# Optimization experiments

Measured on AMD Instinct MI355X. Metric: run time of the kernel, lower is better.

Reference implementation:

```python
import jax, jax.numpy as jnp
import numpy as np

BITS = 4
MAXQ = 15            # 2**BITS - 1
PACK = 32 // BITS    # 8 int4 values per int32
GROUPSIZE = 128
M, K, N = 2048, 4096, 4096
G = K // GROUPSIZE


def setup_inputs() -> dict:
    key = jax.random.key(0)
    k1, k2, k3, k4, k5 = jax.random.split(key, 5)
    x = jax.random.normal(k1, (M, K), dtype=jnp.float32)
    qweight = jax.random.randint(k2, (K // PACK, N), 0, 2147483647, dtype=jnp.int32)
    qzeros = jax.random.randint(k3, (G, N // PACK), 0, 2147483647, dtype=jnp.int32)
    scales = jax.random.uniform(k4, (G, N), dtype=jnp.float32) * 0.01
    g_idx = (jnp.arange(K, dtype=jnp.int32) // GROUPSIZE).astype(jnp.int32)
    bias = jax.random.normal(k5, (N,), dtype=jnp.float32)
    return {"x": x, "qweight": qweight, "qzeros": qzeros,
            "scales": scales, "g_idx": g_idx, "bias": bias}


def _dequantize(qweight, qzeros, scales, g_idx):
    shifts = (jnp.arange(PACK, dtype=jnp.int32) * BITS)
    # unpack weights along K: [K//8, N] -> [K//8, 8, N] -> [K, N]
    w_int = ((qweight[:, None, :] >> shifts[None, :, None]) & MAXQ)
    w_int = w_int.reshape(K, N)
    # unpack zeros along N: [G, N//8] -> [G, N//8, 8] -> [G, N]; kernel adds 1
    z_int = ((qzeros[:, :, None] >> shifts[None, None, :]) & MAXQ) + 1
    z_int = z_int.reshape(G, N)
    # group-wise dequant: W[k, n] = (w - zeros[g_idx[k]]) * scales[g_idx[k]]
    W = (w_int - z_int[g_idx]).astype(jnp.float32) * scales[g_idx]
    return W  # [K, N]


def reference(x, qweight, qzeros, scales, g_idx, bias):
    W = _dequantize(qweight, qzeros, scales, g_idx)
    return x @ W + bias  # [M, N]
```

## Files before the change

### kernel.cpp

```cpp
#include <hip/hip_runtime.h>
#include <hip/hip_bf16.h>
#include <stdint.h>

#define M_DIM 2048
#define K_DIM 4096
#define N_DIM 4096

typedef __attribute__((ext_vector_type(8))) short short8;
typedef __attribute__((ext_vector_type(4))) float f32x4;

#define MFMA __builtin_amdgcn_mfma_f32_16x16x32_bf16

__device__ __forceinline__ uint32_t bf16pk(float a, float b) {
  uint32_t ua = __float_as_uint(a);
  ua = (ua + 0x7FFFu + ((ua >> 16) & 1u)) >> 16;
  uint32_t ub = __float_as_uint(b);
  ub = (ub + 0x7FFFu + ((ub >> 16) & 1u)) >> 16;
  return ua | (ub << 16);
}

__device__ __forceinline__ void glds16(const char* g, char* l) {
  __builtin_amdgcn_global_load_lds((__attribute__((address_space(1))) void*)g,
                                   (__attribute__((address_space(3))) void*)l, 16, 0, 0);
}


__global__ void __launch_bounds__(256) cvt_x_kernel(const float* __restrict__ x,
                                                    char* __restrict__ xImg) {
  const int mt = blockIdx.x >> 6, kt = blockIdx.x & 63;
  const int tid = threadIdx.x;
  const int k8 = tid & 7, rbase = tid >> 3;
  const float* xb = x + (size_t)mt * 256 * K_DIM + kt * 64 + k8 * 8;
  char* ob = xImg + (size_t)(mt * 64 + kt) * 32768 + k8 * 4096;
#pragma unroll
  for (int j = 0; j < 8; ++j) {
    int row = j * 32 + rbase;
    const float* src = xb + (size_t)row * K_DIM;
    float4 f0 = *(const float4*)src;
    float4 f1 = *(const float4*)(src + 4);
    uint4 pk;
    pk.x = bf16pk(f0.x, f0.y);
    pk.y = bf16pk(f0.z, f0.w);
    pk.z = bf16pk(f1.x, f1.y);
    pk.w = bf16pk(f1.z, f1.w);
    *(uint4*)(ob + row * 16) = pk;
  }
}

__global__ void __launch_bounds__(256) deq_w_kernel(const uint32_t* __restrict__ qweight,
                                                    const uint32_t* __restrict__ qzeros,
                                                    const float* __restrict__ scales,
                                                    char* __restrict__ wImg) {
  const int nt = blockIdx.x >> 6, kt = blockIdx.x & 63;
  const int t = threadIdx.x;
  const int n = nt * 256 + t;
  const int g = kt >> 1;
  uint32_t zq = qzeros[g * (N_DIM / 8) + (n >> 3)];
  const int z = (int)((zq >> ((n & 7) * 4)) & 15u) + 1;
  const float s = scales[g * N_DIM + n];
  char* ob = wImg + (size_t)(nt * 64 + kt) * 32768;
#pragma unroll
  for (int slot = 0; slot < 8; ++slot) {
    uint32_t q = qweight[(size_t)(kt * 8 + slot) * N_DIM + n];
    float f[8];
#pragma unroll
    for (int v = 0; v < 8; ++v) {
      int w = (int)((q >> (4 * v)) & 15u);
      f[v] = (float)(w - z) * s;
    }
    uint4 pk;
    pk.x = bf16pk(f[0], f[1]);
    pk.y = bf16pk(f[2], f[3]);
    pk.z = bf16pk(f[4], f[5]);
    pk.w = bf16pk(f[6], f[7]);
    *(uint4*)(ob + slot * 4096 + t * 16) = pk;
  }
}

__global__ void __launch_bounds__(512, 2) gemm_kernel(const char* __restrict__ xImg,
                                                      const char* __restrict__ wImg,
                                                      const float* __restrict__ bias,
                                                      float* __restrict__ out,
                                                      float* __restrict__ part1) {
  __shared__ uint4 ldsv[8192];
  char* lds = (char*)ldsv;
  const int tid = threadIdx.x;
  const int lane = tid & 63, wid = tid >> 6;
  const int wr = wid >> 2, wc = wid & 3;
  const int lr = lane & 15, lk = lane >> 4;

  const int bid = blockIdx.x;
  const int i5 = bid >> 3;
  const int nb = (bid & 7) * 2 + (i5 & 1);
  const int mb = (i5 >> 1) & 7;
  const int ks = i5 >> 4;

  f32x4 acc[8][4];
#pragma unroll
  for (int i = 0; i < 8; ++i)
#pragma unroll
    for (int j = 0; j < 4; ++j) acc[i][j] = f32x4{0.f, 0.f, 0.f, 0.f};

  const char* aT = xImg + (size_t)(mb * 128 + ks * 64) * 16384;
  const char* bT = wImg + (size_t)(nb * 128 + ks * 64) * 16384;

  int aoff[8], boff[4];
#pragma unroll
  for (int i = 0; i < 8; ++i) aoff[i] = lk * 4096 + (wr * 128 + i * 16 + lr) * 16;
#pragma unroll
  for (int j = 0; j < 4; ++j) boff[j] = 16384 + lk * 4096 + (wc * 64 + j * 16 + lr) * 16;

#define STG(src, dstoff)                                                 \
  do {                                                                   \
    glds16((src) + tid * 16, lds + (dstoff) + tid * 16);                 \
    glds16((src) + 8192 + tid * 16, lds + (dstoff) + 8192 + tid * 16);   \
  } while (0)

  STG(aT, 0);                STG(bT, 16384);
  STG(aT + 16384, 32768);    STG(bT + 16384, 32768 + 16384);
  STG(aT + 32768, 65536);    STG(bT + 32768, 65536 + 16384);
  asm volatile("s_waitcnt vmcnt(8)" ::: "memory");
  __builtin_amdgcn_sched_barrier(0);
  __builtin_amdgcn_s_barrier();

  short8 a0 = *(const short8*)(lds + aoff[0]);
  short8 a1 = *(const short8*)(lds + aoff[1]);
  short8 a2 = *(const short8*)(lds + aoff[2]);
  short8 a3 = *(const short8*)(lds + aoff[3]);
  short8 b0 = *(const short8*)(lds + boff[0]);
  short8 b1 = *(const short8*)(lds + boff[1]);

#pragma unroll 4
  for (int t = 0; t < 64; ++t) {
    const char* buf  = lds + (t & 3) * 32768;
    const char* bufn = lds + ((t + 1) & 3) * 32768;
    const int nso = ((t + 3) & 3) * 32768;
    const char* aN = aT + (size_t)(t + 3) * 16384;
    const char* bN = bT + (size_t)(t + 3) * 16384;

    short8 b2 = *(const short8*)(buf + boff[2]);
    short8 b3 = *(const short8*)(buf + boff[3]);
    short8 a4 = *(const short8*)(buf + aoff[4]);
    short8 a5 = *(const short8*)(buf + aoff[5]);
    short8 a6 = *(const short8*)(buf + aoff[6]);
    short8 a7 = *(const short8*)(buf + aoff[7]);
    if (t <= 60) STG(aN, nso);
    __builtin_amdgcn_sched_barrier(0);
    __builtin_amdgcn_s_barrier();
    asm volatile("s_waitcnt lgkmcnt(6)" ::: "memory");
    __builtin_amdgcn_sched_barrier(0);
    __builtin_amdgcn_s_setprio(1);
    acc[0][0] = MFMA(a0, b0, acc[0][0], 0, 0, 0);
    acc[1][0] = MFMA(a1, b0, acc[1][0], 0, 0, 0);
    acc[2][0] = MFMA(a2, b0, acc[2][0], 0, 0, 0);
    acc[3][0] = MFMA(a3, b0, acc[3][0], 0, 0, 0);
    acc[0][1] = MFMA(a0, b1, acc[0][1], 0, 0, 0);
    acc[1][1] = MFMA(a1, b1, acc[1][1], 0, 0, 0);
    acc[2][1] = MFMA(a2, b1, acc[2][1], 0, 0, 0);
    acc[3][1] = MFMA(a3, b1, acc[3][1], 0, 0, 0);
    asm volatile("s_waitcnt lgkmcnt(4)" ::: "memory");
    __builtin_amdgcn_sched_barrier(0);
    acc[0][2] = MFMA(a0, b2, acc[0][2], 0, 0, 0);
    acc[1][2] = MFMA(a1, b2, acc[1][2], 0, 0, 0);
    acc[2][2] = MFMA(a2, b2, acc[2][2], 0, 0, 0);
    acc[3][2] = MFMA(a3, b2, acc[3][2], 0, 0, 0);
    acc[0][3] = MFMA(a0, b3, acc[0][3], 0, 0, 0);
    acc[1][3] = MFMA(a1, b3, acc[1][3], 0, 0, 0);
    acc[2][3] = MFMA(a2, b3, acc[2][3], 0, 0, 0);
    acc[3][3] = MFMA(a3, b3, acc[3][3], 0, 0, 0);
    __builtin_amdgcn_s_setprio(0);
    if (t <= 60)      asm volatile("s_waitcnt vmcnt(6)" ::: "memory");
    else if (t == 61) asm volatile("s_waitcnt vmcnt(4)" ::: "memory");
    else if (t == 62) asm volatile("s_waitcnt vmcnt(0)" ::: "memory");
    __builtin_amdgcn_sched_barrier(0);
    __builtin_amdgcn_s_barrier();
    __builtin_amdgcn_sched_barrier(0);

    short8 na0 = *(const short8*)(bufn + aoff[0]);
    short8 na1 = *(const short8*)(bufn + aoff[1]);
    short8 na2 = *(const short8*)(bufn + aoff[2]);
    short8 na3 = *(const short8*)(bufn + aoff[3]);
    short8 nb0 = *(const short8*)(bufn + boff[0]);
    short8 nb1 = *(const short8*)(bufn + boff[1]);
    if (t <= 60) STG(bN, nso + 16384);
    __builtin_amdgcn_sched_barrier(0);
    __builtin_amdgcn_s_barrier();
    asm volatile("s_waitcnt lgkmcnt(6)" ::: "memory");
    __builtin_amdgcn_sched_barrier(0);
    __builtin_amdgcn_s_setprio(1);
    acc[4][0] = MFMA(a4, b0, acc[4][0], 0, 0, 0);
    acc[5][0] = MFMA(a5, b0, acc[5][0], 0, 0, 0);
    acc[6][0] = MFMA(a6, b0, acc[6][0], 0, 0, 0);
    acc[7][0] = MFMA(a7, b0, acc[7][0], 0, 0, 0);
    acc[4][1] = MFMA(a4, b1, acc[4][1], 0, 0, 0);
    acc[5][1] = MFMA(a5, b1, acc[5][1], 0, 0, 0);
    acc[6][1] = MFMA(a6, b1, acc[6][1], 0, 0, 0);
    acc[7][1] = MFMA(a7, b1, acc[7][1], 0, 0, 0);
    acc[4][2] = MFMA(a4, b2, acc[4][2], 0, 0, 0);
    acc[5][2] = MFMA(a5, b2, acc[5][2], 0, 0, 0);
    acc[6][2] = MFMA(a6, b2, acc[6][2], 0, 0, 0);
    acc[7][2] = MFMA(a7, b2, acc[7][2], 0, 0, 0);
    acc[4][3] = MFMA(a4, b3, acc[4][3], 0, 0, 0);
    acc[5][3] = MFMA(a5, b3, acc[5][3], 0, 0, 0);
    acc[6][3] = MFMA(a6, b3, acc[6][3], 0, 0, 0);
    acc[7][3] = MFMA(a7, b3, acc[7][3], 0, 0, 0);
    __builtin_amdgcn_s_setprio(0);
    __builtin_amdgcn_sched_barrier(0);
    __builtin_amdgcn_s_barrier();
    __builtin_amdgcn_sched_barrier(0);

    a0 = na0; a1 = na1; a2 = na2; a3 = na3; b0 = nb0; b1 = nb1;
  }
#undef STG

  const int colB = nb * 256 + wc * 64 + lr;
  const int rowB = mb * 256 + wr * 128 + lk * 4;
  if (part1 != nullptr) {
    float* dst = ks ? part1 : out;
#pragma unroll
    for (int j = 0; j < 4; ++j) {
      int col = colB + j * 16;
      float bj = (ks == 0) ? bias[col] : 0.f;
#pragma unroll
      for (int i = 0; i < 8; ++i) {
        int row = rowB + i * 16;
#pragma unroll
        for (int r = 0; r < 4; ++r)
          dst[(size_t)(row + r) * N_DIM + col] = acc[i][j][r] + bj;
      }
    }
  } else {
#pragma unroll
    for (int j = 0; j < 4; ++j) {
      int col = colB + j * 16;
      float bj = (ks == 0) ? bias[col] : 0.f;
#pragma unroll
      for (int i = 0; i < 8; ++i) {
        int row = rowB + i * 16;
#pragma unroll
        for (int r = 0; r < 4; ++r)
          atomicAdd(&out[(size_t)(row + r) * N_DIM + col], acc[i][j][r] + bj);
      }
    }
  }
}

__global__ void __launch_bounds__(256) reduce_kernel(float* __restrict__ out,
                                                     const float* __restrict__ part1) {
  int i = blockIdx.x * 256 + threadIdx.x;
  float4 o = ((const float4*)out)[i];
  float4 p = ((const float4*)part1)[i];
  o.x += p.x; o.y += p.y; o.z += p.z; o.w += p.w;
  ((float4*)out)[i] = o;
}

__global__ void fallback_kernel(const float* __restrict__ x, const uint32_t* __restrict__ qweight,
                                const uint32_t* __restrict__ qzeros, const float* __restrict__ scales,
                                const float* __restrict__ bias, float* __restrict__ out) {
  __shared__ float xs[16][17];
  __shared__ float ws[16][17];
  int tx = threadIdx.x, ty = threadIdx.y;
  int col = blockIdx.x * 16 + tx;
  int row = blockIdx.y * 16 + ty;
  float acc = 0.f;
  for (int k0 = 0; k0 < K_DIM; k0 += 16) {
    xs[ty][tx] = x[(size_t)row * K_DIM + k0 + tx];
    int k = k0 + ty;
    int g = k >> 7;
    uint32_t q = qweight[(size_t)(k >> 3) * N_DIM + col];
    int w = (int)((q >> ((k & 7) * 4)) & 15u);
    uint32_t zq = qzeros[g * (N_DIM / 8) + (col >> 3)];
    int z = (int)((zq >> ((col & 7) * 4)) & 15u) + 1;
    ws[ty][tx] = (float)(w - z) * scales[g * N_DIM + col];
    __syncthreads();
#pragma unroll
    for (int kk = 0; kk < 16; ++kk) acc += xs[ty][kk] * ws[kk][tx];
    __syncthreads();
  }
  out[(size_t)row * N_DIM + col] = acc + bias[col];
}

extern "C" void kernel_launch(void* const* d_in, const int* in_sizes, int n_in,
                              void* d_out, int out_size, void* d_ws, size_t ws_size,
                              hipStream_t stream) {
  const float* x = (const float*)d_in[0];
  const uint32_t* qweight = (const uint32_t*)d_in[1];
  const uint32_t* qzeros = (const uint32_t*)d_in[2];
  const float* scales = (const float*)d_in[3];
  const float* bias = (const float*)d_in[5];
  float* out = (float*)d_out;

  const size_t X_IMG = (size_t)8 * 64 * 32768;
  const size_t W_IMG = (size_t)16 * 64 * 32768;
  const size_t PART = (size_t)M_DIM * N_DIM * 4;

  if (ws_size >= X_IMG + W_IMG + PART) {
    char* xImg = (char*)d_ws;
    char* wImg = (char*)d_ws + X_IMG;
    float* part1 = (float*)((char*)d_ws + X_IMG + W_IMG);
    cvt_x_kernel<<<512, 256, 0, stream>>>(x, xImg);
    deq_w_kernel<<<1024, 256, 0, stream>>>(qweight, qzeros, scales, wImg);
    gemm_kernel<<<256, 512, 0, stream>>>((const char*)xImg, (const char*)wImg, bias, out, part1);
    reduce_kernel<<<8192, 256, 0, stream>>>(out, part1);
  } else if (ws_size >= X_IMG + W_IMG) {
    char* xImg = (char*)d_ws;
    char* wImg = (char*)d_ws + X_IMG;
    hipMemsetAsync(out, 0, (size_t)M_DIM * N_DIM * sizeof(float), stream);
    cvt_x_kernel<<<512, 256, 0, stream>>>(x, xImg);
    deq_w_kernel<<<1024, 256, 0, stream>>>(qweight, qzeros, scales, wImg);
    gemm_kernel<<<256, 512, 0, stream>>>((const char*)xImg, (const char*)wImg, bias, out, nullptr);
  } else {
    fallback_kernel<<<dim3(N_DIM / 16, M_DIM / 16), dim3(16, 16), 0, stream>>>(
        x, qweight, qzeros, scales, bias, out);
  }
}
```

Baseline: 100.3 us.

## Shrink GEMM tile to 128x128 with two-wave blocks and double-buffered LDS

The GEMM tile drops from 256x256 with 8 waves to 128x128 with 2 waves per block, launching 1024 blocks instead of 256. The LDS pipeline goes from a 4-stage ring with split A/B staging to a simple 2-stage double buffer with a full vmcnt(0) wait each step. The x-conversion and weight-dequant kernels are re-laid out to match the new 8 KB sub-tile image format. This trades lower data reuse and less latency hiding for more blocks and better CU fill, and risks exposing global load latency.

```diff
diff --git a/kernel.cpp b/kernel.cpp
--- a/kernel.cpp
+++ b/kernel.cpp
@@ -27,23 +27,22 @@
 
 __global__ void __launch_bounds__(256) cvt_x_kernel(const float* __restrict__ x,
                                                     char* __restrict__ xImg) {
-  const int mt = blockIdx.x >> 6, kt = blockIdx.x & 63;
+  const int mt = blockIdx.x >> 6, ktp = blockIdx.x & 63;
   const int tid = threadIdx.x;
-  const int k8 = tid & 7, rbase = tid >> 3;
-  const float* xb = x + (size_t)mt * 256 * K_DIM + kt * 64 + k8 * 8;
-  char* ob = xImg + (size_t)(mt * 64 + kt) * 32768 + k8 * 4096;
-#pragma unroll
-  for (int j = 0; j < 8; ++j) {
-    int row = j * 32 + rbase;
-    const float* src = xb + (size_t)row * K_DIM;
-    float4 f0 = *(const float4*)src;
-    float4 f1 = *(const float4*)(src + 4);
+  const int row = tid & 127, sh = tid >> 7;
+  const int s = ktp * 2 + sh;
+  const float* src = x + (size_t)(mt * 128 + row) * K_DIM + s * 32;
+  char* dst = xImg + (size_t)(mt * 128 + s) * 8192 + row * 16;
+#pragma unroll
+  for (int slot = 0; slot < 4; ++slot) {
+    float4 f0 = *(const float4*)(src + slot * 8);
+    float4 f1 = *(const float4*)(src + slot * 8 + 4);
     uint4 pk;
     pk.x = bf16pk(f0.x, f0.y);
     pk.y = bf16pk(f0.z, f0.w);
     pk.z = bf16pk(f1.x, f1.y);
     pk.w = bf16pk(f1.z, f1.w);
-    *(uint4*)(ob + row * 16) = pk;
+    *(uint4*)(dst + slot * 2048) = pk;
   }
 }
 
@@ -51,49 +50,48 @@
                                                     const uint32_t* __restrict__ qzeros,
                                                     const float* __restrict__ scales,
                                                     char* __restrict__ wImg) {
-  const int nt = blockIdx.x >> 6, kt = blockIdx.x & 63;
-  const int t = threadIdx.x;
-  const int n = nt * 256 + t;
-  const int g = kt >> 1;
-  uint32_t zq = qzeros[g * (N_DIM / 8) + (n >> 3)];
-  const int z = (int)((zq >> ((n & 7) * 4)) & 15u) + 1;
-  const float s = scales[g * N_DIM + n];
-  char* ob = wImg + (size_t)(nt * 64 + kt) * 32768;
-#pragma unroll
-  for (int slot = 0; slot < 8; ++slot) {
-    uint32_t q = qweight[(size_t)(kt * 8 + slot) * N_DIM + n];
+  const int nt = blockIdx.x >> 6, ktp = blockIdx.x & 63;
+  const int tid = threadIdx.x;
+  const int n = tid & 127, sh = tid >> 7;
+  const int s = ktp * 2 + sh;
+  const int g = ktp >> 1;
+  const int gn = nt * 128 + n;
+  uint32_t zq = qzeros[g * (N_DIM / 8) + (gn >> 3)];
+  const int z = (int)((zq >> ((gn & 7) * 4)) & 15u) + 1;
+  const float s_ = scales[g * N_DIM + gn];
+  char* dst = wImg + (size_t)(nt * 128 + s) * 8192 + n * 16;
+#pragma unroll
+  for (int slot = 0; slot < 4; ++slot) {
+    uint32_t q = qweight[(size_t)(s * 4 + slot) * N_DIM + gn];
     float f[8];
 #pragma unroll
     for (int v = 0; v < 8; ++v) {
       int w = (int)((q >> (4 * v)) & 15u);
-      f[v] = (float)(w - z) * s;
+      f[v] = (float)(w - z) * s_;
     }
     uint4 pk;
     pk.x = bf16pk(f[0], f[1]);
     pk.y = bf16pk(f[2], f[3]);
     pk.z = bf16pk(f[4], f[5]);
     pk.w = bf16pk(f[6], f[7]);
-    *(uint4*)(ob + slot * 4096 + t * 16) = pk;
-  }
-}
-
-__global__ void __launch_bounds__(512, 2) gemm_kernel(const char* __restrict__ xImg,
+    *(uint4*)(dst + slot * 2048) = pk;
+  }
+}
+
+__global__ void __launch_bounds__(128, 2) gemm_kernel(const char* __restrict__ xImg,
                                                       const char* __restrict__ wImg,
                                                       const float* __restrict__ bias,
                                                       float* __restrict__ out,
                                                       float* __restrict__ part1) {
-  __shared__ uint4 ldsv[8192];
+  __shared__ uint4 ldsv[2048];
   char* lds = (char*)ldsv;
   const int tid = threadIdx.x;
-  const int lane = tid & 63, wid = tid >> 6;
-  const int wr = wid >> 2, wc = wid & 3;
+  const int lane = tid & 63, wc = tid >> 6;
   const int lr = lane & 15, lk = lane >> 4;
 
   const int bid = blockIdx.x;
-  const int i5 = bid >> 3;
-  const int nb = (bid & 7) * 2 + (i5 & 1);
-  const int mb = (i5 >> 1) & 7;
-  const int ks = i5 >> 4;
+  const int wg = (bid & 7) * 128 + (bid >> 3);
+  const int mb = wg & 15, nb = (wg >> 4) & 31, ks = wg >> 9;
 
   f32x4 acc[8][4];
 #pragma unroll
@@ -101,120 +99,104 @@
 #pragma unroll
     for (int j = 0; j < 4; ++j) acc[i][j] = f32x4{0.f, 0.f, 0.f, 0.f};
 
-  const char* aT = xImg + (size_t)(mb * 128 + ks * 64) * 16384;
-  const char* bT = wImg + (size_t)(nb * 128 + ks * 64) * 16384;
+  const char* aT = xImg + (size_t)(mb * 128 + ks * 64) * 8192;
+  const char* bT = wImg + (size_t)(nb * 128 + ks * 64) * 8192;
 
   int aoff[8], boff[4];
 #pragma unroll
-  for (int i = 0; i < 8; ++i) aoff[i] = lk * 4096 + (wr * 128 + i * 16 + lr) * 16;
-#pragma unroll
-  for (int j = 0; j < 4; ++j) boff[j] = 16384 + lk * 4096 + (wc * 64 + j * 16 + lr) * 16;
-
-#define STG(src, dstoff)                                                 \
+  for (int i = 0; i < 8; ++i) aoff[i] = lk * 2048 + (i * 16 + lr) * 16;
+#pragma unroll
+  for (int j = 0; j < 4; ++j) boff[j] = 8192 + lk * 2048 + (wc * 64 + j * 16 + lr) * 16;
+
+#define STAGE(T, SB)                                                     \
   do {                                                                   \
-    glds16((src) + tid * 16, lds + (dstoff) + tid * 16);                 \
-    glds16((src) + 8192 + tid * 16, lds + (dstoff) + 8192 + tid * 16);   \
+    const char* sA = aT + (size_t)(T) * 8192;                            \
+    const char* sB = bT + (size_t)(T) * 8192;                            \
+    char* dA = lds + (SB);                                               \
+    _Pragma("unroll")                                                    \
+    for (int h = 0; h < 4; ++h) {                                        \
+      glds16(sA + h * 2048 + tid * 16, dA + h * 2048 + tid * 16);        \
+      glds16(sB + h * 2048 + tid * 16, dA + 8192 + h * 2048 + tid * 16); \
+    }                                                                    \
   } while (0)
 
-  STG(aT, 0);                STG(bT, 16384);
-  STG(aT + 16384, 32768);    STG(bT + 16384, 32768 + 16384);
-  STG(aT + 32768, 65536);    STG(bT + 32768, 65536 + 16384);
-  asm volatile("s_waitcnt vmcnt(8)" ::: "memory");
+  STAGE(0, 0);
+  asm volatile("s_waitcnt vmcnt(0)" ::: "memory");
   __builtin_amdgcn_sched_barrier(0);
   __builtin_amdgcn_s_barrier();
 
-  short8 a0 = *(const short8*)(lds + aoff[0]);
-  short8 a1 = *(const short8*)(lds + aoff[1]);
-  short8 a2 = *(const short8*)(lds + aoff[2]);
-  short8 a3 = *(const short8*)(lds + aoff[3]);
-  short8 b0 = *(const short8*)(lds + boff[0]);
-  short8 b1 = *(const short8*)(lds + boff[1]);
-
-#pragma unroll 4
+#pragma unroll 2
   for (int t = 0; t < 64; ++t) {
-    const char* buf  = lds + (t & 3) * 32768;
-    const char* bufn = lds + ((t + 1) & 3) * 32768;
-    const int nso = ((t + 3) & 3) * 32768;
-    const char* aN = aT + (size_t)(t + 3) * 16384;
-    const char* bN = bT + (size_t)(t + 3) * 16384;
-
-    short8 b2 = *(const short8*)(buf + boff[2]);
-    short8 b3 = *(const short8*)(buf + boff[3]);
+    const char* buf = lds + (t & 1) * 16384;
+    if (t < 63) STAGE(t + 1, ((t + 1) & 1) * 16384);
+    __builtin_amdgcn_sched_barrier(0);
+
+    short8 a0 = *(const short8*)(buf + aoff[0]);
+    short8 a1 = *(const short8*)(buf + aoff[1]);
+    short8 a2 = *(const short8*)(buf + aoff[2]);
+    short8 a3 = *(const short8*)(buf + aoff[3]);
     short8 a4 = *(const short8*)(buf + aoff[4]);
     short8 a5 = *(const short8*)(buf + aoff[5]);
     short8 a6 = *(const short8*)(buf + aoff[6]);
     short8 a7 = *(const short8*)(buf + aoff[7]);
-    if (t <= 60) STG(aN, nso);
-    __builtin_amdgcn_sched_barrier(0);
-    __builtin_amdgcn_s_barrier();
-    asm volatile("s_waitcnt lgkmcnt(6)" ::: "memory");
+    short8 b0 = *(const short8*)(buf + boff[0]);
+    short8 b1 = *(const short8*)(buf + boff[1]);
+    short8 b2 = *(const short8*)(buf + boff[2]);
+    short8 b3 = *(const short8*)(buf + boff[3]);
+
+    asm volatile("s_waitcnt lgkmcnt(3)" ::: "memory");
     __builtin_amdgcn_sched_barrier(0);
     __builtin_amdgcn_s_setprio(1);
     acc[0][0] = MFMA(a0, b0, acc[0][0], 0, 0, 0);
     acc[1][0] = MFMA(a1, b0, acc[1][0], 0, 0, 0);
     acc[2][0] = MFMA(a2, b0, acc[2][0], 0, 0, 0);
     acc[3][0] = MFMA(a3, b0, acc[3][0], 0, 0, 0);
+    acc[4][0] = MFMA(a4, b0, acc[4][0], 0, 0, 0);
+    acc[5][0] = MFMA(a5, b0, acc[5][0], 0, 0, 0);
+    acc[6][0] = MFMA(a6, b0, acc[6][0], 0, 0, 0);
+    acc[7][0] = MFMA(a7, b0, acc[7][0], 0, 0, 0);
+    asm volatile("s_waitcnt lgkmcnt(2)" ::: "memory");
+    __builtin_amdgcn_sched_barrier(0);
     acc[0][1] = MFMA(a0, b1, acc[0][1], 0, 0, 0);
     acc[1][1] = MFMA(a1, b1, acc[1][1], 0, 0, 0);
     acc[2][1] = MFMA(a2, b1, acc[2][1], 0, 0, 0);
     acc[3][1] = MFMA(a3, b1, acc[3][1], 0, 0, 0);
-    asm volatile("s_waitcnt lgkmcnt(4)" ::: "memory");
+    acc[4][1] = MFMA(a4, b1, acc[4][1], 0, 0, 0);
+    acc[5][1] = MFMA(a5, b1, acc[5][1], 0, 0, 0);
+    acc[6][1] = MFMA(a6, b1, acc[6][1], 0, 0, 0);
+    acc[7][1] = MFMA(a7, b1, acc[7][1], 0, 0, 0);
+    asm volatile("s_waitcnt lgkmcnt(1)" ::: "memory");
     __builtin_amdgcn_sched_barrier(0);
     acc[0][2] = MFMA(a0, b2, acc[0][2], 0, 0, 0);
     acc[1][2] = MFMA(a1, b2, acc[1][2], 0, 0, 0);
     acc[2][2] = MFMA(a2, b2, acc[2][2], 0, 0, 0);
     acc[3][2] = MFMA(a3, b2, acc[3][2], 0, 0, 0);
+    acc[4][2] = MFMA(a4, b2, acc[4][2], 0, 0, 0);
+    acc[5][2] = MFMA(a5, b2, acc[5][2], 0, 0, 0);
+    acc[6][2] = MFMA(a6, b2, acc[6][2], 0, 0, 0);
+    acc[7][2] = MFMA(a7, b2, acc[7][2], 0, 0, 0);
+    asm volatile("s_waitcnt lgkmcnt(0)" ::: "memory");
+    __builtin_amdgcn_sched_barrier(0);
     acc[0][3] = MFMA(a0, b3, acc[0][3], 0, 0, 0);
     acc[1][3] = MFMA(a1, b3, acc[1][3], 0, 0, 0);
     acc[2][3] = MFMA(a2, b3, acc[2][3], 0, 0, 0);
     acc[3][3] = MFMA(a3, b3, acc[3][3], 0, 0, 0);
-    __builtin_amdgcn_s_setprio(0);
-    if (t <= 60)      asm volatile("s_waitcnt vmcnt(6)" ::: "memory");
-    else if (t == 61) asm volatile("s_waitcnt vmcnt(4)" ::: "memory");
-    else if (t == 62) asm volatile("s_waitcnt vmcnt(0)" ::: "memory");
-    __builtin_amdgcn_sched_barrier(0);
-    __builtin_amdgcn_s_barrier();
-    __builtin_amdgcn_sched_barrier(0);
-
-    short8 na0 = *(const short8*)(bufn + aoff[0]);
-    short8 na1 = *(const short8*)(bufn + aoff[1]);
-    short8 na2 = *(const short8*)(bufn + aoff[2]);
-    short8 na3 = *(const short8*)(bufn + aoff[3]);
-    short8 nb0 = *(const short8*)(bufn + boff[0]);
-    short8 nb1 = *(const short8*)(bufn + boff[1]);
-    if (t <= 60) STG(bN, nso + 16384);
-    __builtin_amdgcn_sched_barrier(0);
-    __builtin_amdgcn_s_barrier();
-    asm volatile("s_waitcnt lgkmcnt(6)" ::: "memory");
-    __builtin_amdgcn_sched_barrier(0);
-    __builtin_amdgcn_s_setprio(1);
-    acc[4][0] = MFMA(a4, b0, acc[4][0], 0, 0, 0);
-    acc[5][0] = MFMA(a5, b0, acc[5][0], 0, 0, 0);
-    acc[6][0] = MFMA(a6, b0, acc[6][0], 0, 0, 0);
-    acc[7][0] = MFMA(a7, b0, acc[7][0], 0, 0, 0);
-    acc[4][1] = MFMA(a4, b1, acc[4][1], 0, 0, 0);
-    acc[5][1] = MFMA(a5, b1, acc[5][1], 0, 0, 0);
-    acc[6][1] = MFMA(a6, b1, acc[6][1], 0, 0, 0);
-    acc[7][1] = MFMA(a7, b1, acc[7][1], 0, 0, 0);
-    acc[4][2] = MFMA(a4, b2, acc[4][2], 0, 0, 0);
-    acc[5][2] = MFMA(a5, b2, acc[5][2], 0, 0, 0);
-    acc[6][2] = MFMA(a6, b2, acc[6][2], 0, 0, 0);
-    acc[7][2] = MFMA(a7, b2, acc[7][2], 0, 0, 0);
     acc[4][3] = MFMA(a4, b3, acc[4][3], 0, 0, 0);
     acc[5][3] = MFMA(a5, b3, acc[5][3], 0, 0, 0);
     acc[6][3] = MFMA(a6, b3, acc[6][3], 0, 0, 0);
     acc[7][3] = MFMA(a7, b3, acc[7][3], 0, 0, 0);
     __builtin_amdgcn_s_setprio(0);
-    __builtin_amdgcn_sched_barrier(0);
-    __builtin_amdgcn_s_barrier();
-    __builtin_amdgcn_sched_barrier(0);
-
-    a0 = na0; a1 = na1; a2 = na2; a3 = na3; b0 = nb0; b1 = nb1;
-  }
-#undef STG
-
-  const int colB = nb * 256 + wc * 64 + lr;
-  const int rowB = mb * 256 + wr * 128 + lk * 4;
+
+    if (t < 63) {
+      asm volatile("s_waitcnt vmcnt(0)" ::: "memory");
+      __builtin_amdgcn_sched_barrier(0);
+      __builtin_amdgcn_s_barrier();
+    }
+  }
+#undef STAGE
+
+  const int colB = nb * 128 + wc * 64 + lr;
+  const int rowB = mb * 128 + lk * 4;
   if (part1 != nullptr) {
     float* dst = ks ? part1 : out;
 #pragma unroll
@@ -290,25 +272,25 @@
   const float* bias = (const float*)d_in[5];
   float* out = (float*)d_out;
 
-  const size_t X_IMG = (size_t)8 * 64 * 32768;
-  const size_t W_IMG = (size_t)16 * 64 * 32768;
+  const size_t X_IMG = (size_t)16 * 128 * 8192;
+  const size_t W_IMG = (size_t)32 * 128 * 8192;
   const size_t PART = (size_t)M_DIM * N_DIM * 4;
 
   if (ws_size >= X_IMG + W_IMG + PART) {
     char* xImg = (char*)d_ws;
     char* wImg = (char*)d_ws + X_IMG;
     float* part1 = (float*)((char*)d_ws + X_IMG + W_IMG);
-    cvt_x_kernel<<<512, 256, 0, stream>>>(x, xImg);
-    deq_w_kernel<<<1024, 256, 0, stream>>>(qweight, qzeros, scales, wImg);
-    gemm_kernel<<<256, 512, 0, stream>>>((const char*)xImg, (const char*)wImg, bias, out, part1);
+    cvt_x_kernel<<<1024, 256, 0, stream>>>(x, xImg);
+    deq_w_kernel<<<2048, 256, 0, stream>>>(qweight, qzeros, scales, wImg);
+    gemm_kernel<<<1024, 128, 0, stream>>>(xImg, wImg, bias, out, part1);
     reduce_kernel<<<8192, 256, 0, stream>>>(out, part1);
   } else if (ws_size >= X_IMG + W_IMG) {
     char* xImg = (char*)d_ws;
     char* wImg = (char*)d_ws + X_IMG;
     hipMemsetAsync(out, 0, (size_t)M_DIM * N_DIM * sizeof(float), stream);
-    cvt_x_kernel<<<512, 256, 0, stream>>>(x, xImg);
-    deq_w_kernel<<<1024, 256, 0, stream>>>(qweight, qzeros, scales, wImg);
-    gemm_kernel<<<256, 512, 0, stream>>>((const char*)xImg, (const char*)wImg, bias, out, nullptr);
+    cvt_x_kernel<<<1024, 256, 0, stream>>>(x, xImg);
+    deq_w_kernel<<<2048, 256, 0, stream>>>(qweight, qzeros, scales, wImg);
+    gemm_kernel<<<1024, 128, 0, stream>>>(xImg, wImg, bias, out, nullptr);
   } else {
     fallback_kernel<<<dim3(N_DIM / 16, M_DIM / 16), dim3(16, 16), 0, stream>>>(
         x, qweight, qzeros, scales, bias, out);
```

After: 101.0 us. About the same (+0.7%).
